# Optimization experiments

Measured on AMD Instinct MI355X. Metric: run time of the kernel, lower is better.

Reference implementation:

```python
import jax, jax.numpy as jnp
import numpy as np

DIM = 1024
NUM_HEADS = 16
HEAD_DIM = DIM // NUM_HEADS
SCALE = HEAD_DIM ** -0.5


def setup_inputs() -> dict:
    key = jax.random.key(0)
    ks = jax.random.split(key, 9)
    s = 1.0 / np.sqrt(DIM)
    x = jax.random.normal(ks[0], (2, 2048, DIM), dtype=jnp.float32)
    Wq = jax.random.normal(ks[1], (DIM, DIM), dtype=jnp.float32) * s
    Wk = jax.random.normal(ks[2], (DIM, DIM), dtype=jnp.float32) * s
    Wv = jax.random.normal(ks[3], (DIM, DIM), dtype=jnp.float32) * s
    Wp = jax.random.normal(ks[4], (DIM, DIM), dtype=jnp.float32) * s
    bq = jax.random.normal(ks[5], (DIM,), dtype=jnp.float32) * s
    bk = jax.random.normal(ks[6], (DIM,), dtype=jnp.float32) * s
    bv = jax.random.normal(ks[7], (DIM,), dtype=jnp.float32) * s
    bp = jax.random.normal(ks[8], (DIM,), dtype=jnp.float32) * s
    return {"x": x, "Wq": Wq, "bq": bq, "Wk": Wk, "bk": bk,
            "Wv": Wv, "bv": bv, "Wp": Wp, "bp": bp}


def reference(x, Wq, bq, Wk, bk, Wv, bv, Wp, bp):
    B, L, C = x.shape
    H, D = NUM_HEADS, HEAD_DIM
    # Linear projections (torch Linear: x @ W.T + b)
    q = x @ Wq.T + bq
    k = x @ Wk.T + bk
    v = x @ Wv.T + bv
    # (B, L, H*D) -> (B, H, L, D)
    q = q.reshape(B, L, H, D).transpose(0, 2, 1, 3)
    k = k.reshape(B, L, H, D).transpose(0, 2, 1, 3)
    v = v.reshape(B, L, H, D).transpose(0, 2, 1, 3)
    # scaled dot-product attention, full L x L scores (as in source)
    attn = jnp.einsum('bhqd,bhkd->bhqk', q, k) * SCALE
    attn = jax.nn.softmax(attn, axis=-1)
    out = jnp.einsum('bhqk,bhkd->bhqd', attn, v)
    out = out.transpose(0, 2, 1, 3).reshape(B, L, C)
    return out @ Wp.T + bp
```

## Files before the change

### kernel.cpp

```cpp
#include <hip/hip_runtime.h>

#define DIMC 1024
#define SEQL 2048
#define NB   2
#define NH   16
#define HD   64
#define MTOT (NB*SEQL)
#define XSTR 2048
static constexpr float SM_SCALE = 0.125f;
static constexpr float LOG2E    = 1.4426950408889634f;
static constexpr float QSCALE   = SM_SCALE * LOG2E;

typedef short s16x8 __attribute__((ext_vector_type(8)));
typedef short s16x4 __attribute__((ext_vector_type(4)));
typedef float f32x4 __attribute__((ext_vector_type(4)));
typedef int   i32x4 __attribute__((ext_vector_type(4)));

__device__ __forceinline__ unsigned short f2bf(float f) {
    unsigned int u = __float_as_uint(f);
    u += 0x7fffu + ((u >> 16) & 1u);
    return (unsigned short)(u >> 16);
}
__device__ __forceinline__ s16x8 ld8(const unsigned short* p) {
    return *(const s16x8*)p;
}
__device__ __forceinline__ void gld_lds16(const unsigned short* g, unsigned short* l) {
    __builtin_amdgcn_global_load_lds(
        (const __attribute__((address_space(1))) void*)g,
        (__attribute__((address_space(3))) void*)l, 16, 0, 0);
}
__device__ __forceinline__ unsigned int cvtpk(float lo, float hi) {
    unsigned int r;
    asm("v_cvt_pk_bf16_f32 %0, %1, %2" : "=v"(r) : "v"(lo), "v"(hi));
    return r;
}

__global__ __launch_bounds__(256) void cast_all(
    const float* __restrict__ x,
    const float* __restrict__ Wq, const float* __restrict__ Wk,
    const float* __restrict__ Wv, const float* __restrict__ Wp,
    const float* __restrict__ bq, const float* __restrict__ bk,
    const float* __restrict__ bvv,
    unsigned short* __restrict__ xb, unsigned short* __restrict__ wall,
    float* __restrict__ ball)
{
    const int bid = blockIdx.x, tid = threadIdx.x;
    if (bid < 4096) {
        int i = bid * 256 + tid;
        float4 f = ((const float4*)x)[i];
        s16x4 o;
        o[0] = (short)f2bf(f.x); o[1] = (short)f2bf(f.y);
        o[2] = (short)f2bf(f.z); o[3] = (short)f2bf(f.w);
        ((s16x4*)xb)[i] = o;
    } else if (bid < 8192) {
        int j = (bid - 4096) * 256 + tid;
        int r = j >> 18;
        const float* src = (r == 0) ? Wq : (r == 1) ? Wk : (r == 2) ? Wv : Wp;
        float4 f = ((const float4*)src)[j & 262143];
        s16x4 o;
        o[0] = (short)f2bf(f.x); o[1] = (short)f2bf(f.y);
        o[2] = (short)f2bf(f.z); o[3] = (short)f2bf(f.w);
        ((s16x4*)wall)[j] = o;
    } else {
        int t2 = (bid - 8192) * 256 + tid;
        if (t2 < 3072)
            ball[t2] = (t2 < 1024) ? bq[t2]
                     : (t2 < 2048) ? bk[t2 - 1024] : bvv[t2 - 2048];
    }
}

__global__ __launch_bounds__(256) void gemm_tile(
    const unsigned short* __restrict__ A, int astride,
    const unsigned short* __restrict__ Wb,
    const float* __restrict__ bias,
    unsigned short* qk, unsigned short* vtb, float* outf, int mode)
{
    __shared__ __align__(16) unsigned short Asm[128 * 32];
    __shared__ __align__(16) unsigned short Bsm[128 * 32];

    const int t    = threadIdx.x;
    const int lane = t & 63;
    const int l15  = lane & 15;
    const int quad = lane >> 4;
    const int w    = t >> 6;
    const int mrow = (w & 1) * 64;
    const int ncol = (w >> 1) * 64;
    const int mt   = blockIdx.x & 31;
    const int nt   = blockIdx.x >> 5;
    const int row0 = mt * 128;

    const unsigned short* ga = A  + (size_t)(row0 + (t >> 2)) * astride + (t & 3) * 8;
    const unsigned short* gb = Wb + (size_t)(nt * 128 + (t >> 2)) * DIMC + (t & 3) * 8;
    const size_t gaStep = (size_t)64 * astride;
    const size_t gbStep = (size_t)64 * DIMC;

    f32x4 acc[4][4] = {};

    for (int k0 = 0; k0 < DIMC; k0 += 32) {
        gld_lds16(ga + k0,          Asm + t * 8);
        gld_lds16(ga + gaStep + k0, Asm + 2048 + t * 8);
        gld_lds16(gb + k0,          Bsm + t * 8);
        gld_lds16(gb + gbStep + k0, Bsm + 2048 + t * 8);
        __syncthreads();

        s16x8 a[4], b[4];
#pragma unroll
        for (int mi = 0; mi < 4; ++mi)
            a[mi] = *(const s16x8*)(Asm + (mrow + mi * 16 + l15) * 32 + quad * 8);
#pragma unroll
        for (int ni = 0; ni < 4; ++ni)
            b[ni] = *(const s16x8*)(Bsm + (ncol + ni * 16 + l15) * 32 + quad * 8);
#pragma unroll
        for (int mi = 0; mi < 4; ++mi)
#pragma unroll
            for (int ni = 0; ni < 4; ++ni)
                acc[mi][ni] = __builtin_amdgcn_mfma_f32_16x16x32_bf16(
                    a[mi], b[ni], acc[mi][ni], 0, 0, 0);
        __syncthreads();
    }

    const int proj = nt >> 3;
#pragma unroll
    for (int ni = 0; ni < 4; ++ni) {
        const int cq = (nt & 7) * 128 + ncol + ni * 16 + l15;
        const float bz = bias[proj * 1024 + cq];
#pragma unroll
        for (int mi = 0; mi < 4; ++mi) {
            const int rbase = row0 + mrow + mi * 16 + quad * 4;
            if (mode == 0) {
                if (proj < 2) {
                    const float scale = (proj == 0) ? QSCALE : 1.0f;
#pragma unroll
                    for (int r = 0; r < 4; ++r)
                        qk[(size_t)(rbase + r) * XSTR + proj * DIMC + cq] =
                            f2bf((acc[mi][ni][r] + bz) * scale);
                } else {
                    const int h = cq >> 6, d = cq & 63;
                    const int bb = rbase >> 11, ll = rbase & (SEQL - 1);
                    s16x4 v4;
                    v4[0] = (short)f2bf(acc[mi][ni][0] + bz);
                    v4[1] = (short)f2bf(acc[mi][ni][1] + bz);
                    v4[2] = (short)f2bf(acc[mi][ni][2] + bz);
                    v4[3] = (short)f2bf(acc[mi][ni][3] + bz);
                    *(s16x4*)(vtb + ((size_t)((bb * NH + h) * HD + d)) * SEQL + ll) = v4;
                }
            } else {
#pragma unroll
                for (int r = 0; r < 4; ++r)
                    outf[(size_t)(rbase + r) * DIMC + cq] = acc[mi][ni][r] + bz;
            }
        }
    }
}

__global__ __launch_bounds__(128) void attn_fused(
    unsigned short* xqk,
    const unsigned short* __restrict__ vt)
{
    __shared__ __align__(16) unsigned short Ksm[2][64 * 64];
    __shared__ __align__(16) unsigned short Vsm[2][64 * 64];

    const int t    = threadIdx.x;
    const int lane = t & 63;
    const int l15  = lane & 15;
    const int quad = lane >> 4;
    const int w    = t >> 6;

    const int xcd = blockIdx.x & 7;
    const int ii  = blockIdx.x >> 3;
    const int bh  = (xcd << 2) | (ii >> 5);
    const int qb  = ii & 31;
    const int h  = bh & (NH - 1);
    const int bb = bh >> 4;
    const int q0A = qb * 64 + w * 16;
    const int q0B = q0A + 32;

    unsigned short* qbase = xqk + (size_t)(bb * SEQL) * XSTR + h * HD + quad * 8;
    unsigned short* qrA = qbase + (size_t)(q0A + l15) * XSTR;
    unsigned short* qrB = qbase + (size_t)(q0B + l15) * XSTR;
    const s16x8 bqA0 = ld8(qrA), bqA1 = ld8(qrA + 32);
    const s16x8 bqB0 = ld8(qrB), bqB1 = ld8(qrB + 32);

    s16x8 bones;
#pragma unroll
    for (int e = 0; e < 8; ++e) bones[e] = (short)0x3F80;

    const int tr = t >> 3, tp = t & 7;
    const int swz = (tp ^ (tr & 7)) * 8;
    const unsigned short* kg = xqk + (size_t)bb * SEQL * XSTR + DIMC + h * HD
                               + (size_t)tr * XSTR + swz;
    const unsigned short* vg = vt + (size_t)(bh * HD + tr) * SEQL + swz;

    f32x4 oA[4] = {}, oB[4] = {};
    f32x4 laccA = {}, laccB = {};
    const int xk = l15 & 7;

#pragma unroll
    for (int g = 0; g < 4; ++g) {
        gld_lds16(kg + (size_t)(g * 16) * XSTR, Ksm[0] + g * 1024 + t * 8);
        gld_lds16(vg + (size_t)(g * 16) * SEQL, Vsm[0] + g * 1024 + t * 8);
    }
    __syncthreads();

    for (int j0 = 0; j0 < SEQL; j0 += 64) {
        const int cur = (j0 >> 6) & 1, nxt = cur ^ 1;
        if (j0 + 64 < SEQL) {
            const int jn = j0 + 64;
#pragma unroll
            for (int g = 0; g < 4; ++g) {
                gld_lds16(kg + (size_t)(jn + g * 16) * XSTR, Ksm[nxt] + g * 1024 + t * 8);
                gld_lds16(vg + (size_t)(g * 16) * SEQL + jn,  Vsm[nxt] + g * 1024 + t * 8);
            }
        }
        const unsigned short* Kc = Ksm[cur];
        const unsigned short* Vc = Vsm[cur];

#pragma unroll
        for (int hf = 0; hf < 2; ++hf) {
            const int k0 = (hf * 32 + l15) * 64;
            const int k1 = (hf * 32 + 16 + l15) * 64;
            s16x8 a00 = *(const s16x8*)(Kc + k0 + ((quad       ^ xk) * 8));
            s16x8 a01 = *(const s16x8*)(Kc + k0 + (((quad + 4) ^ xk) * 8));
            s16x8 a10 = *(const s16x8*)(Kc + k1 + ((quad       ^ xk) * 8));
            s16x8 a11 = *(const s16x8*)(Kc + k1 + (((quad + 4) ^ xk) * 8));

            s16x8 bv[4];
#pragma unroll
            for (int c = 0; c < 4; ++c) {
                const unsigned short* va = Vc + (c * 16 + l15) * 64 + (quad & 1) * 4;
                const int kc0 = hf * 4 + (quad >> 1);
                s16x4 v0 = *(const s16x4*)(va + ((kc0       ^ xk) * 8));
                s16x4 v1 = *(const s16x4*)(va + (((kc0 + 2) ^ xk) * 8));
                bv[c] = __builtin_shufflevector(v0, v1, 0, 1, 2, 3, 4, 5, 6, 7);
            }

            {
                f32x4 st0 = {}, st1 = {};
                st0 = __builtin_amdgcn_mfma_f32_16x16x32_bf16(a00, bqA0, st0, 0, 0, 0);
                st0 = __builtin_amdgcn_mfma_f32_16x16x32_bf16(a01, bqA1, st0, 0, 0, 0);
                st1 = __builtin_amdgcn_mfma_f32_16x16x32_bf16(a10, bqA0, st1, 0, 0, 0);
                st1 = __builtin_amdgcn_mfma_f32_16x16x32_bf16(a11, bqA1, st1, 0, 0, 0);
                i32x4 api;
                api[0] = (int)cvtpk(__builtin_amdgcn_exp2f(st0[0]),
                                    __builtin_amdgcn_exp2f(st0[1]));
                api[1] = (int)cvtpk(__builtin_amdgcn_exp2f(st0[2]),
                                    __builtin_amdgcn_exp2f(st0[3]));
                api[2] = (int)cvtpk(__builtin_amdgcn_exp2f(st1[0]),
                                    __builtin_amdgcn_exp2f(st1[1]));
                api[3] = (int)cvtpk(__builtin_amdgcn_exp2f(st1[2]),
                                    __builtin_amdgcn_exp2f(st1[3]));
                s16x8 ap = __builtin_bit_cast(s16x8, api);
                laccA = __builtin_amdgcn_mfma_f32_16x16x32_bf16(ap, bones, laccA, 0, 0, 0);
#pragma unroll
                for (int c = 0; c < 4; ++c)
                    oA[c] = __builtin_amdgcn_mfma_f32_16x16x32_bf16(ap, bv[c], oA[c], 0, 0, 0);
            }
            {
                f32x4 st0 = {}, st1 = {};
                st0 = __builtin_amdgcn_mfma_f32_16x16x32_bf16(a00, bqB0, st0, 0, 0, 0);
                st0 = __builtin_amdgcn_mfma_f32_16x16x32_bf16(a01, bqB1, st0, 0, 0, 0);
                st1 = __builtin_amdgcn_mfma_f32_16x16x32_bf16(a10, bqB0, st1, 0, 0, 0);
                st1 = __builtin_amdgcn_mfma_f32_16x16x32_bf16(a11, bqB1, st1, 0, 0, 0);
                i32x4 api;
                api[0] = (int)cvtpk(__builtin_amdgcn_exp2f(st0[0]),
                                    __builtin_amdgcn_exp2f(st0[1]));
                api[1] = (int)cvtpk(__builtin_amdgcn_exp2f(st0[2]),
                                    __builtin_amdgcn_exp2f(st0[3]));
                api[2] = (int)cvtpk(__builtin_amdgcn_exp2f(st1[0]),
                                    __builtin_amdgcn_exp2f(st1[1]));
                api[3] = (int)cvtpk(__builtin_amdgcn_exp2f(st1[2]),
                                    __builtin_amdgcn_exp2f(st1[3]));
                s16x8 ap = __builtin_bit_cast(s16x8, api);
                laccB = __builtin_amdgcn_mfma_f32_16x16x32_bf16(ap, bones, laccB, 0, 0, 0);
#pragma unroll
                for (int c = 0; c < 4; ++c)
                    oB[c] = __builtin_amdgcn_mfma_f32_16x16x32_bf16(ap, bv[c], oB[c], 0, 0, 0);
            }
        }
        __syncthreads();
    }

    float liA[4], liB[4];
#pragma unroll
    for (int r = 0; r < 4; ++r) {
        liA[r] = 1.0f / laccA[r];
        liB[r] = 1.0f / laccB[r];
    }

#pragma unroll
    for (int c = 0; c < 4; ++c) {
        const int d = c * 16 + l15;
#pragma unroll
        for (int r = 0; r < 4; ++r) {
            const int qr = quad * 4 + r;
            xqk[(size_t)(bb * SEQL + q0A + qr) * XSTR + h * HD + d] = f2bf(oA[c][r] * liA[r]);
            xqk[(size_t)(bb * SEQL + q0B + qr) * XSTR + h * HD + d] = f2bf(oB[c][r] * liB[r]);
        }
    }
}

extern "C" void kernel_launch(void* const* d_in, const int* in_sizes, int n_in,
                              void* d_out, int out_size, void* d_ws, size_t ws_size,
                              hipStream_t stream) {
    const float* x  = (const float*)d_in[0];
    const float* Wq = (const float*)d_in[1];
    const float* bq = (const float*)d_in[2];
    const float* Wk = (const float*)d_in[3];
    const float* bk = (const float*)d_in[4];
    const float* Wv = (const float*)d_in[5];
    const float* bv = (const float*)d_in[6];
    const float* Wp = (const float*)d_in[7];
    const float* bp = (const float*)d_in[8];
    float* out = (float*)d_out;
    unsigned short* vtb = (unsigned short*)d_out;
    unsigned short* xqk = (unsigned short*)d_in[0];

    unsigned short* ws   = (unsigned short*)d_ws;
    const size_t XELT = (size_t)MTOT * DIMC;
    const size_t WELT = (size_t)DIMC * DIMC;
    unsigned short* xb   = ws;
    unsigned short* wall = ws + XELT;
    float*          ball = (float*)(ws + 2 * XELT);

    cast_all<<<8204, 256, 0, stream>>>(x, Wq, Wk, Wv, Wp, bq, bk, bv, xb, wall, ball);

    gemm_tile<<<768, 256, 0, stream>>>(xb, DIMC, wall, ball, xqk, vtb, nullptr, 0);

    attn_fused<<<NB * NH * (SEQL / 64), 128, 0, stream>>>(xqk, vtb);

    gemm_tile<<<256, 256, 0, stream>>>(xqk, XSTR, wall + 3 * WELT, bp,
                                       nullptr, nullptr, out, 1);
}
```

Measured before the change: 220.7 us.

## Double attention block size, use manual vmcnt waits, XCD-aware GEMM tile mapping

The attention kernel now runs 256 threads per block covering 128 query rows, so each K/V tile is staged in two 32-row chunks per thread and shared by twice as many queries. The loop is unrolled by two with explicit s_waitcnt vmcnt and raw s_barrier in place of __syncthreads, so prefetching the next tile overlaps compute without a full memory drain. MFMA sections are wrapped in s_setprio to favour math waves. The GEMM block index is remapped so each XCD processes a contiguous range of N tiles to improve L2 reuse of weights. The grid halves to 512 attention blocks, which may lower occupancy, and the raw barriers depend on correct vmcnt accounting.

```diff
diff --git a/kernel.cpp b/kernel.cpp
--- a/kernel.cpp
+++ b/kernel.cpp
@@ -34,6 +34,10 @@
     asm("v_cvt_pk_bf16_f32 %0, %1, %2" : "=v"(r) : "v"(lo), "v"(hi));
     return r;
 }
+
+#define BAR()    asm volatile("s_barrier" ::: "memory")
+#define WAITVM4() asm volatile("s_waitcnt vmcnt(4)" ::: "memory")
+#define WAITVM0() asm volatile("s_waitcnt vmcnt(0)" ::: "memory")
 
 __global__ __launch_bounds__(256) void cast_all(
     const float* __restrict__ x,
@@ -85,8 +89,11 @@
     const int w    = t >> 6;
     const int mrow = (w & 1) * 64;
     const int ncol = (w >> 1) * 64;
-    const int mt   = blockIdx.x & 31;
-    const int nt   = blockIdx.x >> 5;
+    const int nt_total = (int)gridDim.x >> 5;
+    const int xcd = blockIdx.x & 7;
+    const int i2  = blockIdx.x >> 3;
+    const int nt  = xcd * (nt_total >> 3) + (i2 >> 5);
+    const int mt  = i2 & 31;
     const int row0 = mt * 128;
 
     const unsigned short* ga = A  + (size_t)(row0 + (t >> 2)) * astride + (t & 3) * 8;
@@ -153,7 +160,7 @@
     }
 }
 
-__global__ __launch_bounds__(128) void attn_fused(
+__global__ __launch_bounds__(256) void attn_fused(
     unsigned short* xqk,
     const unsigned short* __restrict__ vt)
 {
@@ -168,12 +175,12 @@
 
     const int xcd = blockIdx.x & 7;
     const int ii  = blockIdx.x >> 3;
-    const int bh  = (xcd << 2) | (ii >> 5);
-    const int qb  = ii & 31;
+    const int bh  = (xcd << 2) | (ii >> 4);
+    const int qb  = ii & 15;
     const int h  = bh & (NH - 1);
     const int bb = bh >> 4;
-    const int q0A = qb * 64 + w * 16;
-    const int q0B = q0A + 32;
+    const int q0A = qb * 128 + w * 16;
+    const int q0B = q0A + 64;
 
     unsigned short* qbase = xqk + (size_t)(bb * SEQL) * XSTR + h * HD + quad * 8;
     unsigned short* qrA = qbase + (size_t)(q0A + l15) * XSTR;
@@ -195,26 +202,15 @@
     f32x4 laccA = {}, laccB = {};
     const int xk = l15 & 7;
 
-#pragma unroll
-    for (int g = 0; g < 4; ++g) {
-        gld_lds16(kg + (size_t)(g * 16) * XSTR, Ksm[0] + g * 1024 + t * 8);
-        gld_lds16(vg + (size_t)(g * 16) * SEQL, Vsm[0] + g * 1024 + t * 8);
-    }
-    __syncthreads();
-
-    for (int j0 = 0; j0 < SEQL; j0 += 64) {
-        const int cur = (j0 >> 6) & 1, nxt = cur ^ 1;
-        if (j0 + 64 < SEQL) {
-            const int jn = j0 + 64;
-#pragma unroll
-            for (int g = 0; g < 4; ++g) {
-                gld_lds16(kg + (size_t)(jn + g * 16) * XSTR, Ksm[nxt] + g * 1024 + t * 8);
-                gld_lds16(vg + (size_t)(g * 16) * SEQL + jn,  Vsm[nxt] + g * 1024 + t * 8);
-            }
-        }
-        const unsigned short* Kc = Ksm[cur];
-        const unsigned short* Vc = Vsm[cur];
-
+    auto stage = [&](unsigned short* Kb, unsigned short* Vb, int j) {
+#pragma unroll
+        for (int g = 0; g < 2; ++g) {
+            gld_lds16(kg + (size_t)(j + g * 32) * XSTR, Kb + g * 2048 + t * 8);
+            gld_lds16(vg + (size_t)(g * 32) * SEQL + j,  Vb + g * 2048 + t * 8);
+        }
+    };
+
+    auto compute = [&](const unsigned short* Kc, const unsigned short* Vc) {
 #pragma unroll
         for (int hf = 0; hf < 2; ++hf) {
             const int k0 = (hf * 32 + l15) * 64;
@@ -234,6 +230,7 @@
                 bv[c] = __builtin_shufflevector(v0, v1, 0, 1, 2, 3, 4, 5, 6, 7);
             }
 
+            __builtin_amdgcn_s_setprio(1);
             {
                 f32x4 st0 = {}, st1 = {};
                 st0 = __builtin_amdgcn_mfma_f32_16x16x32_bf16(a00, bqA0, st0, 0, 0, 0);
@@ -276,8 +273,29 @@
                 for (int c = 0; c < 4; ++c)
                     oB[c] = __builtin_amdgcn_mfma_f32_16x16x32_bf16(ap, bv[c], oB[c], 0, 0, 0);
             }
-        }
-        __syncthreads();
+            __builtin_amdgcn_s_setprio(0);
+        }
+    };
+
+    stage(Ksm[0], Vsm[0], 0);
+
+#pragma unroll 1
+    for (int jt = 0; jt < SEQL / 64; jt += 2) {
+        const int j0 = jt * 64;
+        stage(Ksm[1], Vsm[1], j0 + 64);
+        WAITVM4();
+        BAR();
+        compute(Ksm[0], Vsm[0]);
+        BAR();
+        if (jt + 2 < SEQL / 64) {
+            stage(Ksm[0], Vsm[0], j0 + 128);
+            WAITVM4();
+        } else {
+            WAITVM0();
+        }
+        BAR();
+        compute(Ksm[1], Vsm[1]);
+        BAR();
     }
 
     float liA[4], liB[4];
@@ -326,7 +344,7 @@
 
     gemm_tile<<<768, 256, 0, stream>>>(xb, DIMC, wall, ball, xqk, vtb, nullptr, 0);
 
-    attn_fused<<<NB * NH * (SEQL / 64), 128, 0, stream>>>(xqk, vtb);
+    attn_fused<<<NB * NH * (SEQL / 128), 256, 0, stream>>>(xqk, vtb);
 
     gemm_tile<<<256, 256, 0, stream>>>(xqk, XSTR, wall + 3 * WELT, bp,
                                        nullptr, nullptr, out, 1);
```

Result: faster. 214.8 us (-2.6%).
